# Performance work log

Measured on AMD Instinct MI355X. Metric: run time of the kernel, lower is better.

## Reference

```python
import jax, jax.numpy as jnp
import numpy as np

B, S, D = 4, 4096, 1024          # batch, seq, d_model
K, H, A = 32, 4, 2               # mem_key_dim, mem_hashes, mem_assoc
T, NB = 65536, 16                # mem_buckets = 2**NB
Dm, Tv = 64, 32                  # mem_dim, mem_vsa_dim
READ_TEMP, VSA_W = 1.0, 1.0
TANH_SCALE, BETA, NOV_THR = 1.0, 1.0, 0.0
WRITE_THR, ETA = 0.5, 0.1


def setup_inputs() -> dict:
    key = jax.random.key(0)
    k = jax.random.split(key, 12)
    s = 0.02
    return {
        "u": jax.random.normal(k[0], (B, S, D), jnp.float32),
        "Wq": jax.random.normal(k[1], (K, D), jnp.float32) * s,
        "Ww": jax.random.normal(k[2], (K, D), jnp.float32) * s,
        "Wv": jax.random.normal(k[3], (Dm, D), jnp.float32) * s,
        "Wout": jax.random.normal(k[4], (D, Dm), jnp.float32) * s,
        "Wg": jax.random.normal(k[5], (1, D), jnp.float32) * s,
        "bg": jnp.zeros((1,), jnp.float32),
        "R": jax.random.normal(k[6], (H, K, NB), jnp.float32),
        "P": jax.random.normal(k[7], (Tv, K), jnp.float32) / np.float32(np.sqrt(K)),
        "mem_keys": jax.random.normal(k[8], (T, A, K), jnp.float32),
        "mem_vals": jax.random.normal(k[9], (T, A, Dm), jnp.float32),
        "mem_tags": jnp.tanh(jax.random.normal(k[10], (T, A, Tv), jnp.float32)),
    }


def reference(u, Wq, Ww, Wv, Wout, Wg, bg, R, P, mem_keys, mem_vals, mem_tags):
    # --- routing (BitRouter): sign bits of random projections -> bucket per hash ---
    q = jnp.einsum('bsd,kd->bsk', u, Wq)                              # query tag
    bits = (jnp.einsum('bsk,hkn->bshn', q, R) > 0).astype(jnp.int32)
    pw = 2 ** jnp.arange(NB, dtype=jnp.int32)
    idx = jnp.sum(bits * pw, axis=-1)                                 # [B,S,H] in [0,T)

    # --- read: gather bucket slots, key + VSA-tag scores, softmax over H*A ---
    Kg, Vg, Tg = mem_keys[idx], mem_vals[idx], mem_tags[idx]          # [B,S,H,A,*]
    score = jnp.einsum('bsk,bshak->bsha', q, Kg) / jnp.sqrt(jnp.float32(K))
    qt = jnp.tanh(TANH_SCALE * jnp.einsum('bsk,tk->bst', q, P))       # VSA tag of query
    score = score + VSA_W * jnp.einsum('bst,bshat->bsha', qt, Tg) / Tv
    attn = jax.nn.softmax((score / READ_TEMP).reshape(B, S, H * A), axis=-1)
    attn = attn.reshape(B, S, H, A)
    read = jnp.einsum('bsha,bshad->bsd', attn, Vg)                    # [B,S,Dm]
    y = jnp.einsum('bsm,dm->bsd', read, Wout)                         # [B,S,D]

    # --- write: gate + VSA novelty, blend best-matching slot, scatter-add ---
    wk = jnp.einsum('bsd,kd->bsk', u, Ww)
    v = jnp.einsum('bsd,md->bsm', u, Wv)
    g = jax.nn.sigmoid(jnp.einsum('bsd,od->bso', u, Wg) + bg)[..., 0]  # [B,S]
    wt = jnp.tanh(TANH_SCALE * jnp.einsum('bsk,tk->bst', wk, P))
    match = jnp.einsum('bst,bshat->bsha', wt, Tg) / Tv
    slot = jnp.argmax(match, axis=-1)                                  # [B,S,H]
    nov = jax.nn.sigmoid(BETA * (NOV_THR - jnp.max(match, axis=-1)))   # novelty gate
    w = ETA * (g * (g > WRITE_THR))[..., None] * nov                   # [B,S,H]
    flat = (idx * A + slot).reshape(-1)                                # [B*S*H]

    def blend(table, gathered, target, dim):
        cur = jnp.take_along_axis(gathered, slot[..., None, None], axis=3)[..., 0, :]
        d = (w[..., None] * (target[:, :, None, :] - cur)).reshape(-1, dim)
        return table.reshape(T * A, dim).at[flat].add(d).reshape(T, A, dim)

    new_keys = blend(mem_keys, Kg, wk, K)
    new_vals = blend(mem_vals, Vg, v, Dm)
    new_tags = blend(mem_tags, Tg, wt, Tv)
    return y, new_keys, new_vals, new_tags
```

## Files before the change

### kernel.cpp

```cpp
#include <hip/hip_runtime.h>
#include <hip/hip_bf16.h>
#include <cstdint>

#define BB 4
#define SS 4096
#define DD 1024
#define KK 32
#define HH 4
#define AA 2
#define TT 65536
#define NBB 16
#define DM 64
#define TV 32
#define MTOK (BB*SS)
#define PKS 4
#define PKL (DD/PKS)

#define WAVE_FENCE() asm volatile("s_waitcnt lgkmcnt(0)" ::: "memory")

__global__ __launch_bounds__(256) void copy_kernel(
    const float* __restrict__ mem_keys, const float* __restrict__ mem_vals,
    const float* __restrict__ mem_tags, float* __restrict__ tab_o)
{
    const size_t NK = (size_t)TT * AA * KK;
    const size_t NV = (size_t)TT * AA * DM;
    const size_t NT = (size_t)TT * AA * TV;
    const size_t total4 = (NK + NV + NT) / 4;
    size_t i = (size_t)blockIdx.x * 256 + threadIdx.x;
    const size_t stride = (size_t)gridDim.x * 256;
    for (; i < total4; i += stride) {
        size_t e = i * 4;
        float4 val;
        if (e < NK)           val = *(const float4*)(mem_keys + e);
        else if (e < NK + NV) val = *(const float4*)(mem_vals + (e - NK));
        else                  val = *(const float4*)(mem_tags + (e - NK - NV));
        *(float4*)(tab_o + e) = val;
    }
}

__global__ __launch_bounds__(256, 2) void proj_kernel(
    const float* __restrict__ u, const float* __restrict__ Wq,
    const float* __restrict__ Ww, const float* __restrict__ Wv,
    const float* __restrict__ Wg,
    float* __restrict__ qs, float* __restrict__ wks,
    float* __restrict__ vs, float* __restrict__ gs)
{
    __shared__ float u_t[128][36];
    __shared__ float w_t[128][36];
    const int t  = threadIdx.x;
    const int mb = blockIdx.x & 127;
    const int ks = blockIdx.x >> 7;
    const int m0 = mb * 128;
    const int kb = ks * PKL;
    const int r0 = t >> 3;
    const int c8 = t & 7;
    const int ty = t >> 4;
    const int tx = t & 15;

    float acc[8][8];
#pragma unroll
    for (int i = 0; i < 8; i++)
#pragma unroll
        for (int j = 0; j < 8; j++) acc[i][j] = 0.f;
    float gp[4] = {0.f, 0.f, 0.f, 0.f};

    for (int k0 = 0; k0 < PKL; k0 += 32) {
        const float4 wg4 = *(const float4*)(Wg + kb + k0 + c8 * 4);
        __syncthreads();
#pragma unroll
        for (int p = 0; p < 4; p++) {
            int r = r0 + 32 * p;
            float4 uv = *(const float4*)(u + (size_t)(m0 + r) * DD + kb + k0 + c8 * 4);
            *(float4*)&u_t[r][c8 * 4] = uv;
            gp[p] = fmaf(uv.x, wg4.x, fmaf(uv.y, wg4.y, fmaf(uv.z, wg4.z, fmaf(uv.w, wg4.w, gp[p]))));
        }
#pragma unroll
        for (int p = 0; p < 4; p++) {
            int c = r0 + 32 * p;
            const float* wrow = (c < 32)  ? (Wq + (size_t)c * DD)
                              : (c < 64)  ? (Ww + (size_t)(c - 32) * DD)
                                          : (Wv + (size_t)(c - 64) * DD);
            *(float4*)&w_t[c][c8 * 4] = *(const float4*)(wrow + kb + k0 + c8 * 4);
        }
        __syncthreads();
#pragma unroll
        for (int k4 = 0; k4 < 8; k4++) {
            float4 a4[8], b4[8];
#pragma unroll
            for (int i = 0; i < 8; i++) a4[i] = *(const float4*)&u_t[ty + 16 * i][k4 * 4];
#pragma unroll
            for (int j = 0; j < 8; j++) b4[j] = *(const float4*)&w_t[tx + 16 * j][k4 * 4];
#pragma unroll
            for (int i = 0; i < 8; i++)
#pragma unroll
                for (int j = 0; j < 8; j++) {
                    acc[i][j] = fmaf(a4[i].x, b4[j].x, acc[i][j]);
                    acc[i][j] = fmaf(a4[i].y, b4[j].y, acc[i][j]);
                    acc[i][j] = fmaf(a4[i].z, b4[j].z, acc[i][j]);
                    acc[i][j] = fmaf(a4[i].w, b4[j].w, acc[i][j]);
                }
        }
    }
#pragma unroll
    for (int p = 0; p < 4; p++) {
        gp[p] += __shfl_xor(gp[p], 1);
        gp[p] += __shfl_xor(gp[p], 2);
        gp[p] += __shfl_xor(gp[p], 4);
    }
    if (c8 == 0) {
#pragma unroll
        for (int p = 0; p < 4; p++) gs[(size_t)ks * MTOK + m0 + r0 + 32 * p] = gp[p];
    }
#pragma unroll
    for (int i = 0; i < 8; i++) {
        int row = m0 + ty + 16 * i;
#pragma unroll
        for (int j = 0; j < 8; j++) {
            if (j < 2)      qs[(size_t)ks * MTOK * KK + (size_t)row * KK + tx + 16 * j]        = acc[i][j];
            else if (j < 4) wks[(size_t)ks * MTOK * KK + (size_t)row * KK + tx + 16 * (j - 2)] = acc[i][j];
            else            vs[(size_t)ks * MTOK * DM + (size_t)row * DM + tx + 16 * (j - 4)]  = acc[i][j];
        }
    }
}

__global__ __launch_bounds__(256) void route_kernel(
    const float* __restrict__ R, const float* __restrict__ P,
    const float* __restrict__ mem_keys, const float* __restrict__ mem_vals,
    const float* __restrict__ mem_tags, const float* __restrict__ bg,
    const float* __restrict__ qs, const float* __restrict__ wks,
    const float* __restrict__ vsl, const float* __restrict__ gsl,
    float* __restrict__ read_o,
    float* __restrict__ keys_o, float* __restrict__ vals_o, float* __restrict__ tags_o)
{
    __shared__ float R_s[4 * 528];
    __shared__ float P_s[TV][KK + 1];
    __shared__ float q_s[4][KK], wk_s[4][KK], qt_s[4][TV], wt_s[4][TV];
    __shared__ float kg_s[4][8][KK], tg_s[4][8][TV], vg_s[4][8][DM];
    __shared__ float sc_s[4][8], mt_s[4][8];
    __shared__ float w_s[4][HH];
    __shared__ int   idx_s[4][HH], slot_s[4][HH];

    const int t    = threadIdx.x;
    const int wid  = t >> 6;
    const int lane = t & 63;

    for (int e = t; e < 2048; e += 256) R_s[(e >> 9) * 528 + (e & 511)] = R[e];
    for (int e = t; e < TV * KK; e += 256) P_s[e >> 5][e & 31] = P[e];
    const float bgv = bg[0];
    __syncthreads();

    for (int ti = 0; ti < 4; ti++) {
        const int tok = blockIdx.x * 16 + wid * 4 + ti;
        if (lane < 32) {
            float s = 0.f;
#pragma unroll
            for (int sl = 0; sl < PKS; sl++) s += qs[(size_t)sl * MTOK * KK + (size_t)tok * KK + lane];
            q_s[wid][lane] = s;
        } else {
            int l2 = lane - 32;
            float s = 0.f;
#pragma unroll
            for (int sl = 0; sl < PKS; sl++) s += wks[(size_t)sl * MTOK * KK + (size_t)tok * KK + l2];
            wk_s[wid][l2] = s;
        }
        WAVE_FENCE();
        {
            int h = lane >> 4, n = lane & 15;
            float s = 0.f;
#pragma unroll
            for (int k = 0; k < KK; k++) s = fmaf(q_s[wid][k], R_s[h * 528 + k * 16 + n], s);
            unsigned long long m = __ballot(s > 0.f);
            if (n == 0) idx_s[wid][h] = (int)((m >> (h * 16)) & 0xFFFFull);
        }
        if (lane < 32) {
            float s = 0.f;
#pragma unroll
            for (int k = 0; k < KK; k++) s = fmaf(q_s[wid][k], P_s[lane][k], s);
            qt_s[wid][lane] = tanhf(s);
        } else {
            int t2 = lane - 32;
            float s = 0.f;
#pragma unroll
            for (int k = 0; k < KK; k++) s = fmaf(wk_s[wid][k], P_s[t2][k], s);
            wt_s[wid][t2] = tanhf(s);
        }
        WAVE_FENCE();
        {
            int p = lane >> 3, j = lane & 7;
            int h = p >> 1, a = p & 1;
            size_t sb = (size_t)idx_s[wid][h] * AA + a;
            *(float4*)&kg_s[wid][p][j * 4] = *(const float4*)(mem_keys + sb * KK + j * 4);
            *(float4*)&tg_s[wid][p][j * 4] = *(const float4*)(mem_tags + sb * TV + j * 4);
            *(float4*)&vg_s[wid][p][j * 8]     = *(const float4*)(mem_vals + sb * DM + j * 8);
            *(float4*)&vg_s[wid][p][j * 8 + 4] = *(const float4*)(mem_vals + sb * DM + j * 8 + 4);
        }
        WAVE_FENCE();
        if (lane < 8) {
            int p = lane;
            float s1 = 0.f, s2 = 0.f;
#pragma unroll
            for (int k = 0; k < KK; k++) s1 = fmaf(q_s[wid][k], kg_s[wid][p][k], s1);
#pragma unroll
            for (int k = 0; k < TV; k++) s2 = fmaf(qt_s[wid][k], tg_s[wid][p][k], s2);
            sc_s[wid][p] = s1 * 0.17677669529663688f + s2 * (1.0f / 32.0f);
        } else if (lane < 16) {
            int p = lane - 8;
            float s2 = 0.f;
#pragma unroll
            for (int k = 0; k < TV; k++) s2 = fmaf(wt_s[wid][k], tg_s[wid][p][k], s2);
            mt_s[wid][p] = s2 * (1.0f / 32.0f);
        }
        WAVE_FENCE();
        {
            float sc[8];
#pragma unroll
            for (int p = 0; p < 8; p++) sc[p] = sc_s[wid][p];
            float mx = sc[0];
#pragma unroll
            for (int p = 1; p < 8; p++) mx = fmaxf(mx, sc[p]);
            float e[8], den = 0.f;
#pragma unroll
            for (int p = 0; p < 8; p++) { e[p] = expf(sc[p] - mx); den += e[p]; }
            float inv = 1.f / den;
            float r = 0.f;
#pragma unroll
            for (int p = 0; p < 8; p++) r = fmaf(e[p] * inv, vg_s[wid][p][lane], r);
            read_o[(size_t)tok * DM + lane] = r;
        }
        if (lane < HH) {
            int h = lane;
            float m0v = mt_s[wid][h * 2], m1v = mt_s[wid][h * 2 + 1];
            int sl = (m1v > m0v) ? 1 : 0;
            float mm = fmaxf(m0v, m1v);
            float nov = 1.f / (1.f + expf(mm));
            float gd = bgv;
#pragma unroll
            for (int s2 = 0; s2 < PKS; s2++) gd += gsl[(size_t)s2 * MTOK + tok];
            float gg = 1.f / (1.f + expf(-gd));
            float wv = (gg > 0.5f) ? (0.1f * gg * nov) : 0.f;
            slot_s[wid][h] = sl;
            w_s[wid][h] = wv;
        }
        WAVE_FENCE();
        if (w_s[wid][0] != 0.f) {
            float vsum = 0.f;
#pragma unroll
            for (int sl = 0; sl < PKS; sl++) vsum += vsl[(size_t)sl * MTOK * DM + (size_t)tok * DM + lane];
            int h = lane >> 4, c = lane & 15;
            float wv = w_s[wid][h];
            int sl8 = slot_s[wid][h];
            size_t flat = (size_t)idx_s[wid][h] * AA + sl8;
            int p = h * 2 + sl8;
#pragma unroll
            for (int m = 0; m < 2; m++) {
                int cc = c + 16 * m;
                atomicAdd(keys_o + flat * KK + cc, wv * (wk_s[wid][cc] - kg_s[wid][p][cc]));
                atomicAdd(tags_o + flat * TV + cc, wv * (wt_s[wid][cc] - tg_s[wid][p][cc]));
            }
#pragma unroll
            for (int m = 0; m < 4; m++) {
                int cc = c + 16 * m;
                float vv = __shfl(vsum, cc);
                atomicAdd(vals_o + flat * DM + cc, wv * (vv - vg_s[wid][p][cc]));
            }
        }
        WAVE_FENCE();
    }
}

__global__ __launch_bounds__(256, 2) void ygemm_kernel(
    const float* __restrict__ read_i, const float* __restrict__ Wout,
    float* __restrict__ y_o)
{
    __shared__ float rd_t[128][36];
    __shared__ float wo_t[128][36];
    const int t  = threadIdx.x;
    const int m0 = blockIdx.x * 128;
    const int n0 = blockIdx.y * 128;
    const int r0 = t >> 3;
    const int c8 = t & 7;
    const int ty = t >> 4;
    const int tx = t & 15;

    float acc[8][8];
#pragma unroll
    for (int i = 0; i < 8; i++)
#pragma unroll
        for (int j = 0; j < 8; j++) acc[i][j] = 0.f;

    for (int k0 = 0; k0 < DM; k0 += 32) {
        __syncthreads();
#pragma unroll
        for (int p = 0; p < 4; p++) {
            int r = r0 + 32 * p;
            *(float4*)&rd_t[r][c8 * 4] = *(const float4*)(read_i + (size_t)(m0 + r) * DM + k0 + c8 * 4);
            *(float4*)&wo_t[r][c8 * 4] = *(const float4*)(Wout  + (size_t)(n0 + r) * DM + k0 + c8 * 4);
        }
        __syncthreads();
#pragma unroll
        for (int k4 = 0; k4 < 8; k4++) {
            float4 a4[8], b4[8];
#pragma unroll
            for (int i = 0; i < 8; i++) a4[i] = *(const float4*)&rd_t[ty + 16 * i][k4 * 4];
#pragma unroll
            for (int j = 0; j < 8; j++) b4[j] = *(const float4*)&wo_t[tx + 16 * j][k4 * 4];
#pragma unroll
            for (int i = 0; i < 8; i++)
#pragma unroll
                for (int j = 0; j < 8; j++) {
                    acc[i][j] = fmaf(a4[i].x, b4[j].x, acc[i][j]);
                    acc[i][j] = fmaf(a4[i].y, b4[j].y, acc[i][j]);
                    acc[i][j] = fmaf(a4[i].z, b4[j].z, acc[i][j]);
                    acc[i][j] = fmaf(a4[i].w, b4[j].w, acc[i][j]);
                }
        }
    }
#pragma unroll
    for (int i = 0; i < 8; i++) {
        size_t row = (size_t)(m0 + ty + 16 * i) * DD + n0;
#pragma unroll
        for (int j = 0; j < 8; j++) y_o[row + tx + 16 * j] = acc[i][j];
    }
}

extern "C" void kernel_launch(void* const* d_in, const int* in_sizes, int n_in,
                              void* d_out, int out_size, void* d_ws, size_t ws_size,
                              hipStream_t stream)
{
    (void)in_sizes; (void)n_in; (void)out_size; (void)ws_size;
    const float* u    = (const float*)d_in[0];
    const float* Wq   = (const float*)d_in[1];
    const float* Ww   = (const float*)d_in[2];
    const float* Wv   = (const float*)d_in[3];
    const float* Wout = (const float*)d_in[4];
    const float* Wg   = (const float*)d_in[5];
    const float* bg   = (const float*)d_in[6];
    const float* R    = (const float*)d_in[7];
    const float* P    = (const float*)d_in[8];
    const float* mem_keys = (const float*)d_in[9];
    const float* mem_vals = (const float*)d_in[10];
    const float* mem_tags = (const float*)d_in[11];

    float* y_o    = (float*)d_out;
    float* keys_o = y_o    + (size_t)MTOK * DD;
    float* vals_o = keys_o + (size_t)TT * AA * KK;
    float* tags_o = vals_o + (size_t)TT * AA * DM;

    float* qs  = y_o;
    float* wks = qs  + (size_t)PKS * MTOK * KK;
    float* vsl = wks + (size_t)PKS * MTOK * KK;
    float* gsl = vsl + (size_t)PKS * MTOK * DM;

    float* read_w = (float*)d_ws;

    copy_kernel<<<2048, 256, 0, stream>>>(mem_keys, mem_vals, mem_tags, keys_o);
    proj_kernel<<<128 * PKS, 256, 0, stream>>>(u, Wq, Ww, Wv, Wg, qs, wks, vsl, gsl);
    route_kernel<<<MTOK / 16, 256, 0, stream>>>(R, P, mem_keys, mem_vals, mem_tags, bg,
                                                qs, wks, vsl, gsl, read_w,
                                                keys_o, vals_o, tags_o);
    ygemm_kernel<<<dim3(MTOK / 128, DD / 128), 256, 0, stream>>>(read_w, Wout, y_o);
}
```

Before: 369.9 us.

## Fuse table copy into projection kernel, prefetch tiles, vectorize y stores

Merges the memory-table copy kernel into the projection GEMM launch, with odd blocks doing the copy and even blocks the GEMM, so copy bandwidth overlaps with compute and one launch is dropped. Both GEMMs now prefetch the next K-tile into registers while the current tile is computed. The route kernel hoists the q/wk partial-sum loads and the v partial sums ahead of the dependent compute. The y GEMM remaps its columns so output rows are written with float4 stores. These changes raise register pressure and change the mix of work resident on the GPU at once.

```diff
diff --git a/kernel.cpp b/kernel.cpp
--- a/kernel.cpp
+++ b/kernel.cpp
@@ -18,38 +18,38 @@
 
 #define WAVE_FENCE() asm volatile("s_waitcnt lgkmcnt(0)" ::: "memory")
 
-__global__ __launch_bounds__(256) void copy_kernel(
-    const float* __restrict__ mem_keys, const float* __restrict__ mem_vals,
-    const float* __restrict__ mem_tags, float* __restrict__ tab_o)
-{
-    const size_t NK = (size_t)TT * AA * KK;
-    const size_t NV = (size_t)TT * AA * DM;
-    const size_t NT = (size_t)TT * AA * TV;
-    const size_t total4 = (NK + NV + NT) / 4;
-    size_t i = (size_t)blockIdx.x * 256 + threadIdx.x;
-    const size_t stride = (size_t)gridDim.x * 256;
-    for (; i < total4; i += stride) {
-        size_t e = i * 4;
-        float4 val;
-        if (e < NK)           val = *(const float4*)(mem_keys + e);
-        else if (e < NK + NV) val = *(const float4*)(mem_vals + (e - NK));
-        else                  val = *(const float4*)(mem_tags + (e - NK - NV));
-        *(float4*)(tab_o + e) = val;
-    }
-}
-
-__global__ __launch_bounds__(256, 2) void proj_kernel(
+__global__ __launch_bounds__(256, 2) void proj_copy_kernel(
     const float* __restrict__ u, const float* __restrict__ Wq,
     const float* __restrict__ Ww, const float* __restrict__ Wv,
     const float* __restrict__ Wg,
+    const float* __restrict__ mem_keys, const float* __restrict__ mem_vals,
+    const float* __restrict__ mem_tags, float* __restrict__ tab_o,
     float* __restrict__ qs, float* __restrict__ wks,
     float* __restrict__ vs, float* __restrict__ gs)
 {
     __shared__ float u_t[128][36];
     __shared__ float w_t[128][36];
-    const int t  = threadIdx.x;
-    const int mb = blockIdx.x & 127;
-    const int ks = blockIdx.x >> 7;
+    const int t = threadIdx.x;
+
+    if (blockIdx.x & 1) {
+        const size_t NK = (size_t)TT * AA * KK;
+        const size_t NV = (size_t)TT * AA * DM;
+        const size_t base = (size_t)(blockIdx.x >> 1) * 8192 + t;
+#pragma unroll
+        for (int m = 0; m < 32; m++) {
+            size_t e = (base + (size_t)m * 256) * 4;
+            float4 val;
+            if (e < NK)           val = *(const float4*)(mem_keys + e);
+            else if (e < NK + NV) val = *(const float4*)(mem_vals + (e - NK));
+            else                  val = *(const float4*)(mem_tags + (e - NK - NV));
+            *(float4*)(tab_o + e) = val;
+        }
+        return;
+    }
+
+    const int cb = blockIdx.x >> 1;
+    const int mb = cb & 127;
+    const int ks = cb >> 7;
     const int m0 = mb * 128;
     const int kb = ks * PKL;
     const int r0 = t >> 3;
@@ -64,23 +64,47 @@
         for (int j = 0; j < 8; j++) acc[i][j] = 0.f;
     float gp[4] = {0.f, 0.f, 0.f, 0.f};
 
-    for (int k0 = 0; k0 < PKL; k0 += 32) {
-        const float4 wg4 = *(const float4*)(Wg + kb + k0 + c8 * 4);
-        __syncthreads();
-#pragma unroll
-        for (int p = 0; p < 4; p++) {
-            int r = r0 + 32 * p;
-            float4 uv = *(const float4*)(u + (size_t)(m0 + r) * DD + kb + k0 + c8 * 4);
-            *(float4*)&u_t[r][c8 * 4] = uv;
-            gp[p] = fmaf(uv.x, wg4.x, fmaf(uv.y, wg4.y, fmaf(uv.z, wg4.z, fmaf(uv.w, wg4.w, gp[p]))));
-        }
+    float4 ur[4], wr[4], wg4;
+    {
+        int kc = kb;
+#pragma unroll
+        for (int p = 0; p < 4; p++)
+            ur[p] = *(const float4*)(u + (size_t)(m0 + r0 + 32 * p) * DD + kc + c8 * 4);
 #pragma unroll
         for (int p = 0; p < 4; p++) {
             int c = r0 + 32 * p;
             const float* wrow = (c < 32)  ? (Wq + (size_t)c * DD)
                               : (c < 64)  ? (Ww + (size_t)(c - 32) * DD)
                                           : (Wv + (size_t)(c - 64) * DD);
-            *(float4*)&w_t[c][c8 * 4] = *(const float4*)(wrow + kb + k0 + c8 * 4);
+            wr[p] = *(const float4*)(wrow + kc + c8 * 4);
+        }
+        wg4 = *(const float4*)(Wg + kc + c8 * 4);
+    }
+
+    for (int it = 0; it < 8; ++it) {
+        if (it) __syncthreads();
+#pragma unroll
+        for (int p = 0; p < 4; p++) {
+            int r = r0 + 32 * p;
+            *(float4*)&u_t[r][c8 * 4] = ur[p];
+            gp[p] = fmaf(ur[p].x, wg4.x, fmaf(ur[p].y, wg4.y,
+                     fmaf(ur[p].z, wg4.z, fmaf(ur[p].w, wg4.w, gp[p]))));
+            *(float4*)&w_t[r][c8 * 4] = wr[p];
+        }
+        if (it < 7) {
+            int kc = kb + (it + 1) * 32;
+#pragma unroll
+            for (int p = 0; p < 4; p++)
+                ur[p] = *(const float4*)(u + (size_t)(m0 + r0 + 32 * p) * DD + kc + c8 * 4);
+#pragma unroll
+            for (int p = 0; p < 4; p++) {
+                int c = r0 + 32 * p;
+                const float* wrow = (c < 32)  ? (Wq + (size_t)c * DD)
+                                  : (c < 64)  ? (Ww + (size_t)(c - 32) * DD)
+                                              : (Wv + (size_t)(c - 64) * DD);
+                wr[p] = *(const float4*)(wrow + kc + c8 * 4);
+            }
+            wg4 = *(const float4*)(Wg + kc + c8 * 4);
         }
         __syncthreads();
 #pragma unroll
@@ -147,22 +171,29 @@
     for (int e = t; e < 2048; e += 256) R_s[(e >> 9) * 528 + (e & 511)] = R[e];
     for (int e = t; e < TV * KK; e += 256) P_s[e >> 5][e & 31] = P[e];
     const float bgv = bg[0];
+
+    float qw[4];
+    {
+        const int l2 = lane & 31;
+        const float* src = (lane < 32) ? qs : wks;
+#pragma unroll
+        for (int ti = 0; ti < 4; ti++) {
+            const int tok = blockIdx.x * 16 + wid * 4 + ti;
+            float s = 0.f;
+#pragma unroll
+            for (int sl = 0; sl < PKS; sl++) s += src[(size_t)sl * MTOK * KK + (size_t)tok * KK + l2];
+            qw[ti] = s;
+        }
+    }
     __syncthreads();
 
     for (int ti = 0; ti < 4; ti++) {
         const int tok = blockIdx.x * 16 + wid * 4 + ti;
-        if (lane < 32) {
-            float s = 0.f;
-#pragma unroll
-            for (int sl = 0; sl < PKS; sl++) s += qs[(size_t)sl * MTOK * KK + (size_t)tok * KK + lane];
-            q_s[wid][lane] = s;
-        } else {
-            int l2 = lane - 32;
-            float s = 0.f;
-#pragma unroll
-            for (int sl = 0; sl < PKS; sl++) s += wks[(size_t)sl * MTOK * KK + (size_t)tok * KK + l2];
-            wk_s[wid][l2] = s;
-        }
+        if (lane < 32) q_s[wid][lane] = qw[ti];
+        else           wk_s[wid][lane - 32] = qw[ti];
+        float vsum = 0.f;
+#pragma unroll
+        for (int sl = 0; sl < PKS; sl++) vsum += vsl[(size_t)sl * MTOK * DM + (size_t)tok * DM + lane];
         WAVE_FENCE();
         {
             int h = lane >> 4, n = lane & 15;
@@ -243,9 +274,6 @@
         }
         WAVE_FENCE();
         if (w_s[wid][0] != 0.f) {
-            float vsum = 0.f;
-#pragma unroll
-            for (int sl = 0; sl < PKS; sl++) vsum += vsl[(size_t)sl * MTOK * DM + (size_t)tok * DM + lane];
             int h = lane >> 4, c = lane & 15;
             float wv = w_s[wid][h];
             int sl8 = slot_s[wid][h];
@@ -288,13 +316,28 @@
 #pragma unroll
         for (int j = 0; j < 8; j++) acc[i][j] = 0.f;
 
-    for (int k0 = 0; k0 < DM; k0 += 32) {
-        __syncthreads();
+    float4 rr[4], wwr[4];
+#pragma unroll
+    for (int p = 0; p < 4; p++) {
+        int r = r0 + 32 * p;
+        rr[p]  = *(const float4*)(read_i + (size_t)(m0 + r) * DM + c8 * 4);
+        wwr[p] = *(const float4*)(Wout  + (size_t)(n0 + r) * DM + c8 * 4);
+    }
+    for (int it = 0; it < 2; ++it) {
+        if (it) __syncthreads();
 #pragma unroll
         for (int p = 0; p < 4; p++) {
             int r = r0 + 32 * p;
-            *(float4*)&rd_t[r][c8 * 4] = *(const float4*)(read_i + (size_t)(m0 + r) * DM + k0 + c8 * 4);
-            *(float4*)&wo_t[r][c8 * 4] = *(const float4*)(Wout  + (size_t)(n0 + r) * DM + k0 + c8 * 4);
+            *(float4*)&rd_t[r][c8 * 4] = rr[p];
+            *(float4*)&wo_t[r][c8 * 4] = wwr[p];
+        }
+        if (it == 0) {
+#pragma unroll
+            for (int p = 0; p < 4; p++) {
+                int r = r0 + 32 * p;
+                rr[p]  = *(const float4*)(read_i + (size_t)(m0 + r) * DM + 32 + c8 * 4);
+                wwr[p] = *(const float4*)(Wout  + (size_t)(n0 + r) * DM + 32 + c8 * 4);
+            }
         }
         __syncthreads();
 #pragma unroll
@@ -303,7 +346,7 @@
 #pragma unroll
             for (int i = 0; i < 8; i++) a4[i] = *(const float4*)&rd_t[ty + 16 * i][k4 * 4];
 #pragma unroll
-            for (int j = 0; j < 8; j++) b4[j] = *(const float4*)&wo_t[tx + 16 * j][k4 * 4];
+            for (int j = 0; j < 8; j++) b4[j] = *(const float4*)&wo_t[(j >> 2) * 64 + tx * 4 + (j & 3)][k4 * 4];
 #pragma unroll
             for (int i = 0; i < 8; i++)
 #pragma unroll
@@ -318,8 +361,8 @@
 #pragma unroll
     for (int i = 0; i < 8; i++) {
         size_t row = (size_t)(m0 + ty + 16 * i) * DD + n0;
-#pragma unroll
-        for (int j = 0; j < 8; j++) y_o[row + tx + 16 * j] = acc[i][j];
+        *(float4*)&y_o[row + tx * 4]      = make_float4(acc[i][0], acc[i][1], acc[i][2], acc[i][3]);
+        *(float4*)&y_o[row + 64 + tx * 4] = make_float4(acc[i][4], acc[i][5], acc[i][6], acc[i][7]);
     }
 }
 
@@ -353,8 +396,9 @@
 
     float* read_w = (float*)d_ws;
 
-    copy_kernel<<<2048, 256, 0, stream>>>(mem_keys, mem_vals, mem_tags, keys_o);
-    proj_kernel<<<128 * PKS, 256, 0, stream>>>(u, Wq, Ww, Wv, Wg, qs, wks, vsl, gsl);
+    proj_copy_kernel<<<1024, 256, 0, stream>>>(u, Wq, Ww, Wv, Wg,
+                                               mem_keys, mem_vals, mem_tags, keys_o,
+                                               qs, wks, vsl, gsl);
     route_kernel<<<MTOK / 16, 256, 0, stream>>>(R, P, mem_keys, mem_vals, mem_tags, bg,
                                                 qs, wks, vsl, gsl, read_w,
                                                 keys_o, vals_o, tags_o);
```

Result: slower. 453.3 us (+22.5%).
